# Optimization experiments

Measured on AMD Instinct MI355X. Metric: run time of the kernel, lower is better.

The kernel has to match this reference:

```python
import jax, jax.numpy as jnp
import numpy as np

HEADS = 12
DIM_HEAD = 64
SCALE = DIM_HEAD ** -0.5


def setup_inputs() -> dict:
    key = jax.random.key(0)
    ks = jax.random.split(key, 7)
    b, n, dim = 16, 1024, 768
    inner = HEADS * DIM_HEAD
    x = jax.random.normal(ks[0], (b, n, dim), dtype=jnp.float32)
    Wq = jax.random.normal(ks[1], (dim, inner), dtype=jnp.float32) * (dim ** -0.5)
    Wkv = jax.random.normal(ks[2], (dim, 2 * inner), dtype=jnp.float32) * (dim ** -0.5)
    mix_pre = jax.random.normal(ks[3], (HEADS, HEADS), dtype=jnp.float32)
    mix_post = jax.random.normal(ks[4], (HEADS, HEADS), dtype=jnp.float32)
    Wo = jax.random.normal(ks[5], (inner, dim), dtype=jnp.float32) * (inner ** -0.5)
    bo = jnp.zeros((dim,), dtype=jnp.float32)
    return {"x": x, "Wq": Wq, "Wkv": Wkv, "mix_pre": mix_pre,
            "mix_post": mix_post, "Wo": Wo, "bo": bo}


def reference(x, Wq, Wkv, mix_pre, mix_post, Wo, bo):
    b, n, dim = x.shape
    h, d = HEADS, DIM_HEAD
    # projections (context is None -> context = x)
    q = (x @ Wq).reshape(b, n, h, d).transpose(0, 2, 1, 3)        # b h n d
    kv = x @ Wkv
    k = kv[..., : h * d].reshape(b, n, h, d).transpose(0, 2, 1, 3)
    v = kv[..., h * d:].reshape(b, n, h, d).transpose(0, 2, 1, 3)
    # scaled QK^T
    attn = jnp.einsum('bhid,bhjd->bhij', q, k) * SCALE             # b h n n
    # talking-heads pre-softmax: mix over head dim
    attn = jnp.einsum('bhij,hg->bgij', attn, mix_pre)
    attn = jax.nn.softmax(attn, axis=-1)
    # talking-heads post-softmax
    attn = jnp.einsum('bhij,hg->bgij', attn, mix_post)
    out = jnp.einsum('bhij,bhjd->bhid', attn, v)                   # b h n d
    out = out.transpose(0, 2, 1, 3).reshape(b, n, h * d)           # b n (h d)
    return out @ Wo + bo
```

## Files before the change

kernel.cpp:

```cpp
#include <hip/hip_runtime.h>


typedef _Float16 f16;
typedef _Float16 f16x8 __attribute__((ext_vector_type(8)));
typedef _Float16 f16x4 __attribute__((ext_vector_type(4)));
typedef float f32x4 __attribute__((ext_vector_type(4)));
typedef float fv4 __attribute__((ext_vector_type(4)));

#define MFMA(a, b, c) __builtin_amdgcn_mfma_f32_16x16x32_f16(a, b, c, 0, 0, 0)
#define MFMA16(a, b, c) __builtin_amdgcn_mfma_f32_16x16x16f16(a, b, c, 0, 0, 0)

__global__ __launch_bounds__(256) void k_cast_x(const float* __restrict__ x,
                                                f16* __restrict__ xb) {
  int idx = (blockIdx.x * 256 + threadIdx.x) * 8;
  fv4 a = *(const fv4*)(x + idx);
  fv4 b = *(const fv4*)(x + idx + 4);
  f16x8 o;
  o[0] = (f16)a[0]; o[1] = (f16)a[1]; o[2] = (f16)a[2]; o[3] = (f16)a[3];
  o[4] = (f16)b[0]; o[5] = (f16)b[1]; o[6] = (f16)b[2]; o[7] = (f16)b[3];
  *(f16x8*)(xb + idx) = o;
}

__global__ __launch_bounds__(256) void k_prep_w(const float* __restrict__ Wq,
                                                const float* __restrict__ Wkv,
                                                const float* __restrict__ Wo,
                                                f16* __restrict__ Wt,
                                                f16* __restrict__ WoT) {
  int idx = blockIdx.x * 256 + threadIdx.x;
  if (idx < 2304 * 768) {
    int n = idx / 768, k = idx % 768;
    float v = (n < 768) ? Wq[k * 768 + n] * 0.125f
                        : Wkv[k * 1536 + (n - 768)];
    Wt[idx] = (f16)v;
  } else {
    int id2 = idx - 2304 * 768;
    int n = id2 / 768, k = id2 % 768;
    WoT[id2] = (f16)Wo[k * 768 + n];
  }
}

__global__ __launch_bounds__(256) void k_gemm_qkv(const f16* __restrict__ A,
                                                  const f16* __restrict__ Bt,
                                                  f16* __restrict__ qb,
                                                  f16* __restrict__ kb,
                                                  f16* __restrict__ vb) {
  __shared__ f16 As[128 * 72];
  __shared__ f16 Bs[128 * 72];
  const int tid = threadIdx.x;
  const int m0 = blockIdx.y << 7;
  const int n0 = blockIdx.x << 7;
  const int lane = tid & 63, w = tid >> 6;
  const int quad = lane >> 4, col = lane & 15;
  const int wm = (w >> 1) << 6, wn = (w & 1) << 6;
  const f32x4 z4 = {0.f, 0.f, 0.f, 0.f};
  f32x4 acc[4][4];
#pragma unroll
  for (int i = 0; i < 4; ++i)
#pragma unroll
    for (int j = 0; j < 4; ++j) acc[i][j] = z4;

  for (int k0 = 0; k0 < 768; k0 += 64) {
#pragma unroll
    for (int s = 0; s < 4; ++s) {
      int u = s * 256 + tid;
      int row = u >> 3, seg = (u & 7) << 3;
      *(f16x8*)&As[row * 72 + seg] = *(const f16x8*)(A + (m0 + row) * 768 + k0 + seg);
      *(f16x8*)&Bs[row * 72 + seg] = *(const f16x8*)(Bt + (n0 + row) * 768 + k0 + seg);
    }
    __syncthreads();
#pragma unroll
    for (int kk = 0; kk < 64; kk += 32) {
      f16x8 af[4], bf[4];
#pragma unroll
      for (int ic = 0; ic < 4; ++ic)
        af[ic] = *(f16x8*)&As[(wm + ic * 16 + col) * 72 + kk + quad * 8];
#pragma unroll
      for (int jc = 0; jc < 4; ++jc)
        bf[jc] = *(f16x8*)&Bs[(wn + jc * 16 + col) * 72 + kk + quad * 8];
#pragma unroll
      for (int ic = 0; ic < 4; ++ic)
#pragma unroll
        for (int jc = 0; jc < 4; ++jc) acc[ic][jc] = MFMA(af[ic], bf[jc], acc[ic][jc]);
    }
    __syncthreads();
  }
#pragma unroll
  for (int jc = 0; jc < 4; ++jc) {
    int gn = n0 + wn + jc * 16 + col;
#pragma unroll
    for (int ic = 0; ic < 4; ++ic)
#pragma unroll
      for (int r = 0; r < 4; ++r) {
        int gm = m0 + wm + ic * 16 + (quad << 2) + r;
        int b = gm >> 10, i = gm & 1023;
        f16 v = (f16)acc[ic][jc][r];
        if (gn < 768) {
          int h = gn >> 6, dd = gn & 63;
          qb[(((b * 12 + h) << 10) + i) * 64 + dd] = v;
        } else if (gn < 1536) {
          int t = gn - 768; int h = t >> 6, dd = t & 63;
          kb[(((b * 12 + h) << 10) + i) * 64 + dd] = v;
        } else {
          int t = gn - 1536; int h = t >> 6, dd = t & 63;
          vb[(((b * 12 + h) << 10) + i) * 64 + dd] = v;
        }
      }
  }
}

__global__ __launch_bounds__(256) void k_transpose_v(const f16* __restrict__ vb,
                                                     f16* __restrict__ vt) {
  __shared__ f16 t[64 * 72];
  const int bh = blockIdx.x;
  const int n0 = blockIdx.y << 6;
  const int tid = threadIdx.x;
#pragma unroll
  for (int s = 0; s < 2; ++s) {
    int u = s * 256 + tid;
    int r = u >> 3, c = (u & 7) << 3;
    *(f16x8*)&t[r * 72 + c] = *(const f16x8*)(vb + (bh * 1024 + n0 + r) * 64 + c);
  }
  __syncthreads();
#pragma unroll
  for (int s = 0; s < 2; ++s) {
    int u = s * 256 + tid;
    int d = u >> 3, c = (u & 7) << 3;
    f16x8 o;
#pragma unroll
    for (int e = 0; e < 8; ++e) o[e] = t[(c + e) * 72 + d];
    *(f16x8*)(vt + (bh * 64 + d) * 1024 + n0 + c) = o;
  }
}

__global__ __launch_bounds__(256, 2) void k_attn(
    const f16* __restrict__ qb, const f16* __restrict__ kb, const f16* __restrict__ vt,
    const float* __restrict__ mixp, const float* __restrict__ mixq,
    f16* __restrict__ ob) {
  extern __shared__ f16 smem[];
  f16* Qs   = smem;
  f16* Slds = smem + 12288;
  f16* Pmb  = smem + 25088;

  const int tid = threadIdx.x;
  const int bid0 = blockIdx.x;
  const int xcd = bid0 & 7, idx = bid0 >> 3;
  const int b = ((idx >> 6) << 3) | xcd;
  const int i0 = (idx & 63) << 4;
  const int lane = tid & 63;
  const int w = tid >> 6;
  const int quad = lane >> 4, col = lane & 15;
  const int q4 = quad << 2;
  const int w3 = w * 3;
  const int jw = w << 4;
  const f32x4 z4 = {0.f, 0.f, 0.f, 0.f};

  f16x4 b_pre, b_post;
#pragma unroll
  for (int e = 0; e < 4; ++e) {
    int hk = q4 + e;
    bool ok = (hk < 12) && (col < 12);
    b_pre[e]  = ok ? (f16)mixp[hk * 12 + col] : (f16)0.f;
    b_post[e] = ok ? (f16)mixq[hk * 12 + col] : (f16)0.f;
  }

  f16* Sw = &Slds[w * 3200];
  if (lane < 16) {
    f16x4 z; z[0] = (f16)0.f; z[1] = (f16)0.f; z[2] = (f16)0.f; z[3] = (f16)0.f;
    *(f16x4*)&Sw[3072 + lane * 4] = z;
  }

#pragma unroll
  for (int s = 0; s < 6; ++s) {
    int u = s * 256 + tid;
    int h = u >> 7, i = (u >> 3) & 15, uu = u & 7;
    f16x8 q = *(const f16x8*)(qb + ((((b * 12 + h) << 10) + i0 + i) << 6) + uu * 8);
    *(f16x8*)&Qs[(((h << 4) + i) << 6) + ((uu ^ (i & 7)) << 3)] = q;
  }
  __syncthreads();

  auto stage = [&](int j0) {
#pragma unroll
    for (int hg = 0; hg < 3; ++hg) {
      f16x8 kr[4][2];
#pragma unroll
      for (int e = 0; e < 4; ++e) {
        const f16* kbase = kb + ((((b * 12 + hg * 4 + e) << 10) + j0 + jw + col) << 6);
        kr[e][0] = *(const f16x8*)(kbase + quad * 8);
        kr[e][1] = *(const f16x8*)(kbase + 32 + quad * 8);
      }
      f32x4 s4[4];
#pragma unroll
      for (int e = 0; e < 4; ++e) {
        int h = hg * 4 + e;
        f16x8 q0 = *(const f16x8*)&Qs[(((h << 4) + col) << 6) +
                                      ((quad ^ (col & 7)) << 3)];
        f16x8 q1 = *(const f16x8*)&Qs[(((h << 4) + col) << 6) +
                                      (((4 + quad) ^ (col & 7)) << 3)];
        f32x4 a = MFMA(q0, kr[e][0], z4);
        s4[e] = MFMA(q1, kr[e][1], a);
      }
#pragma unroll
      for (int r = 0; r < 4; ++r) {
        f16x4 p;
        p[0] = (f16)s4[0][r]; p[1] = (f16)s4[1][r];
        p[2] = (f16)s4[2][r]; p[3] = (f16)s4[3][r];
        *(f16x4*)&Sw[col * 192 + hg * 64 + ((q4 + r + col) & 15) * 4] = p;
      }
    }
  };
  auto sread = [&](int t) -> f16x4 {
    int zi = (quad < 3) ? (t * 192 + quad * 64 + ((col + t) & 15) * 4)
                        : (3072 + ((col + t) & 15) * 4);
    return *(const f16x4*)&Sw[zi];
  };

  float l_run[4] = {0.f, 0.f, 0.f, 0.f};
  for (int j0 = 0; j0 < 1024; j0 += 64) {
    stage(j0);
#pragma unroll
    for (int t = 0; t < 16; ++t) {
      f16x4 sB = sread(t);
      f32x4 d1 = MFMA16(b_pre, sB, z4);
#pragma unroll
      for (int r = 0; r < 4; ++r) l_run[r] += __expf(d1[r]);
    }
  }
  float* Lb = (float*)Pmb;
#pragma unroll
  for (int r = 0; r < 4; ++r) Lb[(w * 16 + q4 + r) * 16 + col] = l_run[r];
  __syncthreads();
  float il[4];
#pragma unroll
  for (int r = 0; r < 4; ++r) {
    float s = 0.f;
#pragma unroll
    for (int ww = 0; ww < 4; ++ww) s += Lb[(ww * 16 + q4 + r) * 16 + col];
    il[r] = 1.f / s;
  }
  __syncthreads();

  f32x4 oa[3][4];
#pragma unroll
  for (int g = 0; g < 3; ++g)
#pragma unroll
    for (int dc = 0; dc < 4; ++dc) oa[g][dc] = z4;

  for (int j0 = 0; j0 < 1024; j0 += 64) {
    stage(j0);
#pragma unroll
    for (int tt = 0; tt < 4; ++tt) {
      f16x4 pk[4];
#pragma unroll
      for (int t4 = 0; t4 < 4; ++t4) {
        int t = tt * 4 + t4;
        f16x4 sB = sread(t);
        f32x4 d1 = MFMA16(b_pre, sB, z4);
        f16x4 pA;
#pragma unroll
        for (int r = 0; r < 4; ++r) pA[r] = (f16)(__expf(d1[r]) * il[r]);
        f32x4 d2 = MFMA16(pA, b_post, z4);
#pragma unroll
        for (int r = 0; r < 4; ++r) pk[r][t4] = (f16)d2[r];
      }
      if (col < 12) {
#pragma unroll
        for (int r = 0; r < 4; ++r) {
          int k4 = (col + q4 + r) & 15;
          *(f16x4*)&Pmb[(((col << 4) + q4 + r) * 16 + ((w * 4 + tt) ^ k4)) * 4] = pk[r];
        }
      }
    }
    __syncthreads();
    __builtin_amdgcn_s_setprio(1);
#pragma unroll
    for (int gg = 0; gg < 3; ++gg) {
      int gp = w3 + gg;
      f16x8 vr[2][4];
#pragma unroll
      for (int jh = 0; jh < 2; ++jh)
#pragma unroll
        for (int dc = 0; dc < 4; ++dc)
          vr[jh][dc] = *(const f16x8*)(vt + ((((b * 12 + gp) << 6) + dc * 16 + col) << 10) +
                                       j0 + jh * 32 + quad * 8);
      int k4r = (gp + col) & 15;
#pragma unroll
      for (int jh = 0; jh < 2; ++jh) {
        int ub = (jh * 4 + quad) * 2;
        f16x4 lo = *(const f16x4*)&Pmb[(((gp << 4) + col) * 16 + (ub ^ k4r)) * 4];
        f16x4 hi = *(const f16x4*)&Pmb[(((gp << 4) + col) * 16 + ((ub + 1) ^ k4r)) * 4];
        f16x8 aP = __builtin_shufflevector(lo, hi, 0, 1, 2, 3, 4, 5, 6, 7);
#pragma unroll
        for (int dc = 0; dc < 4; ++dc)
          oa[gg][dc] = MFMA(aP, vr[jh][dc], oa[gg][dc]);
      }
    }
    __builtin_amdgcn_s_setprio(0);
    __syncthreads();
  }

#pragma unroll
  for (int gg = 0; gg < 3; ++gg) {
    int gp = w3 + gg;
#pragma unroll
    for (int dc = 0; dc < 4; ++dc)
#pragma unroll
      for (int r = 0; r < 4; ++r)
        ob[((b << 10) + i0 + q4 + r) * 768 + gp * 64 + dc * 16 + col] =
            (f16)oa[gg][dc][r];
  }
}

__global__ __launch_bounds__(256) void k_gemm_out(const f16* __restrict__ A,
                                                  const f16* __restrict__ Bt,
                                                  const float* __restrict__ bias,
                                                  float* __restrict__ out) {
  __shared__ f16 As[128 * 72];
  __shared__ f16 Bs[128 * 72];
  const int tid = threadIdx.x;
  const int m0 = blockIdx.y << 7;
  const int n0 = blockIdx.x << 7;
  const int lane = tid & 63, w = tid >> 6;
  const int quad = lane >> 4, col = lane & 15;
  const int wm = (w >> 1) << 6, wn = (w & 1) << 6;
  const f32x4 z4 = {0.f, 0.f, 0.f, 0.f};
  f32x4 acc[4][4];
#pragma unroll
  for (int i = 0; i < 4; ++i)
#pragma unroll
    for (int j = 0; j < 4; ++j) acc[i][j] = z4;

  for (int k0 = 0; k0 < 768; k0 += 64) {
#pragma unroll
    for (int s = 0; s < 4; ++s) {
      int u = s * 256 + tid;
      int row = u >> 3, seg = (u & 7) << 3;
      *(f16x8*)&As[row * 72 + seg] = *(const f16x8*)(A + (m0 + row) * 768 + k0 + seg);
      *(f16x8*)&Bs[row * 72 + seg] = *(const f16x8*)(Bt + (n0 + row) * 768 + k0 + seg);
    }
    __syncthreads();
#pragma unroll
    for (int kk = 0; kk < 64; kk += 32) {
      f16x8 af[4], bf[4];
#pragma unroll
      for (int ic = 0; ic < 4; ++ic)
        af[ic] = *(f16x8*)&As[(wm + ic * 16 + col) * 72 + kk + quad * 8];
#pragma unroll
      for (int jc = 0; jc < 4; ++jc)
        bf[jc] = *(f16x8*)&Bs[(wn + jc * 16 + col) * 72 + kk + quad * 8];
#pragma unroll
      for (int ic = 0; ic < 4; ++ic)
#pragma unroll
        for (int jc = 0; jc < 4; ++jc) acc[ic][jc] = MFMA(af[ic], bf[jc], acc[ic][jc]);
    }
    __syncthreads();
  }
#pragma unroll
  for (int jc = 0; jc < 4; ++jc) {
    int gn = n0 + wn + jc * 16 + col;
    float bv = bias[gn];
#pragma unroll
    for (int ic = 0; ic < 4; ++ic)
#pragma unroll
      for (int r = 0; r < 4; ++r) {
        int gm = m0 + wm + ic * 16 + (quad << 2) + r;
        out[gm * 768 + gn] = acc[ic][jc][r] + bv;
      }
  }
}

extern "C" void kernel_launch(void* const* d_in, const int* in_sizes, int n_in,
                              void* d_out, int out_size, void* d_ws, size_t ws_size,
                              hipStream_t stream) {
  const float* x    = (const float*)d_in[0];
  const float* Wq   = (const float*)d_in[1];
  const float* Wkv  = (const float*)d_in[2];
  const float* mixp = (const float*)d_in[3];
  const float* mixq = (const float*)d_in[4];
  const float* Wo   = (const float*)d_in[5];
  const float* bo   = (const float*)d_in[6];
  float* out = (float*)d_out;

  char* ws = (char*)d_ws;
  f16* xb  = (f16*)(ws);
  f16* Wt  = (f16*)(ws + 25165824);
  f16* WoT = (f16*)(ws + 28704768);
  f16* qb  = (f16*)(ws + 29884416);
  f16* kb  = (f16*)(ws + 55050240);
  f16* vb  = (f16*)(ws + 80216064);
  f16* vt  = xb;
  f16* obuf = vb;

  k_cast_x<<<dim3(6144), dim3(256), 0, stream>>>(x, xb);
  k_prep_w<<<dim3(9216), dim3(256), 0, stream>>>(Wq, Wkv, Wo, Wt, WoT);
  k_gemm_qkv<<<dim3(18, 128), dim3(256), 0, stream>>>(xb, Wt, qb, kb, vb);
  k_transpose_v<<<dim3(192, 16), dim3(256), 0, stream>>>(vb, vt);
  k_attn<<<dim3(1024), dim3(256), 74752, stream>>>(qb, kb, vt, mixp, mixq, obuf);
  k_gemm_out<<<dim3(6, 128), dim3(256), 0, stream>>>(obuf, WoT, bo, out);
}
```

Measured before the change: 773.0 us.

## Prefetch next K tile into registers and double-buffer V loads in attention

Loads for all 12 heads of the next K tile are issued right after the current S tile is computed, so global latency overlaps the softmax and PV work instead of stalling at each stage. S-tile LDS reads are batched up front, and V loads for consecutive heads are double-buffered so each head's PV MFMAs overlap the next head's V fetch. The s_setprio hints are removed. Keeping 24 f16x8 K registers plus two V buffers raises VGPR pressure sharply, which could lower occupancy or cause spills.

Result: slower. 868.4 us (+12.3%).

```diff
diff --git a/kernel.cpp b/kernel.cpp
--- a/kernel.cpp
+++ b/kernel.cpp
@@ -178,16 +178,18 @@
   }
   __syncthreads();
 
-  auto stage = [&](int j0) {
+  f16x8 kr[12][2];
+  auto loadK = [&](int j0) {
+#pragma unroll
+    for (int h = 0; h < 12; ++h) {
+      const f16* kbase = kb + ((((b * 12 + h) << 10) + j0 + jw + col) << 6);
+      kr[h][0] = *(const f16x8*)(kbase + quad * 8);
+      kr[h][1] = *(const f16x8*)(kbase + 32 + quad * 8);
+    }
+  };
+  auto computeS = [&]() {
 #pragma unroll
     for (int hg = 0; hg < 3; ++hg) {
-      f16x8 kr[4][2];
-#pragma unroll
-      for (int e = 0; e < 4; ++e) {
-        const f16* kbase = kb + ((((b * 12 + hg * 4 + e) << 10) + j0 + jw + col) << 6);
-        kr[e][0] = *(const f16x8*)(kbase + quad * 8);
-        kr[e][1] = *(const f16x8*)(kbase + 32 + quad * 8);
-      }
       f32x4 s4[4];
 #pragma unroll
       for (int e = 0; e < 4; ++e) {
@@ -196,8 +198,8 @@
                                       ((quad ^ (col & 7)) << 3)];
         f16x8 q1 = *(const f16x8*)&Qs[(((h << 4) + col) << 6) +
                                       (((4 + quad) ^ (col & 7)) << 3)];
-        f32x4 a = MFMA(q0, kr[e][0], z4);
-        s4[e] = MFMA(q1, kr[e][1], a);
+        f32x4 a = MFMA(q0, kr[h][0], z4);
+        s4[e] = MFMA(q1, kr[h][1], a);
       }
 #pragma unroll
       for (int r = 0; r < 4; ++r) {
@@ -215,12 +217,16 @@
   };
 
   float l_run[4] = {0.f, 0.f, 0.f, 0.f};
+  loadK(0);
   for (int j0 = 0; j0 < 1024; j0 += 64) {
-    stage(j0);
+    computeS();
+    if (j0 + 64 < 1024) loadK(j0 + 64);
+    f16x4 sB[16];
+#pragma unroll
+    for (int t = 0; t < 16; ++t) sB[t] = sread(t);
 #pragma unroll
     for (int t = 0; t < 16; ++t) {
-      f16x4 sB = sread(t);
-      f32x4 d1 = MFMA16(b_pre, sB, z4);
+      f32x4 d1 = MFMA16(b_pre, sB[t], z4);
 #pragma unroll
       for (int r = 0; r < 4; ++r) l_run[r] += __expf(d1[r]);
     }
@@ -245,16 +251,44 @@
 #pragma unroll
     for (int dc = 0; dc < 4; ++dc) oa[g][dc] = z4;
 
+  f16x8 vrA[2][4], vrB[2][4];
+  auto loadV = [&](f16x8 (&vr)[2][4], int gp, int j0) {
+#pragma unroll
+    for (int jh = 0; jh < 2; ++jh)
+#pragma unroll
+      for (int dc = 0; dc < 4; ++dc)
+        vr[jh][dc] = *(const f16x8*)(vt + ((((b * 12 + gp) << 6) + dc * 16 + col) << 10) +
+                                     j0 + jh * 32 + quad * 8);
+  };
+  auto pvHead = [&](f16x8 (&vr)[2][4], int gg) {
+    int gp = w3 + gg;
+    int k4r = (gp + col) & 15;
+#pragma unroll
+    for (int jh = 0; jh < 2; ++jh) {
+      int ub = (jh * 4 + quad) * 2;
+      f16x4 lo = *(const f16x4*)&Pmb[(((gp << 4) + col) * 16 + (ub ^ k4r)) * 4];
+      f16x4 hi = *(const f16x4*)&Pmb[(((gp << 4) + col) * 16 + ((ub + 1) ^ k4r)) * 4];
+      f16x8 aP = __builtin_shufflevector(lo, hi, 0, 1, 2, 3, 4, 5, 6, 7);
+#pragma unroll
+      for (int dc = 0; dc < 4; ++dc)
+        oa[gg][dc] = MFMA(aP, vr[jh][dc], oa[gg][dc]);
+    }
+  };
+
+  loadK(0);
   for (int j0 = 0; j0 < 1024; j0 += 64) {
-    stage(j0);
+    computeS();
+    if (j0 + 64 < 1024) loadK(j0 + 64);
+    f16x4 sB[16];
+#pragma unroll
+    for (int t = 0; t < 16; ++t) sB[t] = sread(t);
 #pragma unroll
     for (int tt = 0; tt < 4; ++tt) {
       f16x4 pk[4];
 #pragma unroll
       for (int t4 = 0; t4 < 4; ++t4) {
         int t = tt * 4 + t4;
-        f16x4 sB = sread(t);
-        f32x4 d1 = MFMA16(b_pre, sB, z4);
+        f32x4 d1 = MFMA16(b_pre, sB[t], z4);
         f16x4 pA;
 #pragma unroll
         for (int r = 0; r < 4; ++r) pA[r] = (f16)(__expf(d1[r]) * il[r]);
@@ -271,30 +305,12 @@
       }
     }
     __syncthreads();
-    __builtin_amdgcn_s_setprio(1);
-#pragma unroll
-    for (int gg = 0; gg < 3; ++gg) {
-      int gp = w3 + gg;
-      f16x8 vr[2][4];
-#pragma unroll
-      for (int jh = 0; jh < 2; ++jh)
-#pragma unroll
-        for (int dc = 0; dc < 4; ++dc)
-          vr[jh][dc] = *(const f16x8*)(vt + ((((b * 12 + gp) << 6) + dc * 16 + col) << 10) +
-                                       j0 + jh * 32 + quad * 8);
-      int k4r = (gp + col) & 15;
-#pragma unroll
-      for (int jh = 0; jh < 2; ++jh) {
-        int ub = (jh * 4 + quad) * 2;
-        f16x4 lo = *(const f16x4*)&Pmb[(((gp << 4) + col) * 16 + (ub ^ k4r)) * 4];
-        f16x4 hi = *(const f16x4*)&Pmb[(((gp << 4) + col) * 16 + ((ub + 1) ^ k4r)) * 4];
-        f16x8 aP = __builtin_shufflevector(lo, hi, 0, 1, 2, 3, 4, 5, 6, 7);
-#pragma unroll
-        for (int dc = 0; dc < 4; ++dc)
-          oa[gg][dc] = MFMA(aP, vr[jh][dc], oa[gg][dc]);
-      }
-    }
-    __builtin_amdgcn_s_setprio(0);
+    loadV(vrA, w3 + 0, j0);
+    loadV(vrB, w3 + 1, j0);
+    pvHead(vrA, 0);
+    loadV(vrA, w3 + 2, j0);
+    pvHead(vrB, 1);
+    pvHead(vrA, 2);
     __syncthreads();
   }
 
```
